# Optimization experiments

Measured on AMD Instinct MI355X. Metric: run time of the kernel, lower is better.

## Reference

```python
import jax, jax.numpy as jnp
import numpy as np

D_MODEL = 1024
NUM_HEADS = 16
HEAD_DIM = D_MODEL // NUM_HEADS  # 64
THETA = 10000.0
B, S = 2, 2048


def setup_inputs() -> dict:
    key = jax.random.key(0)
    k1, k2, k3 = jax.random.split(key, 3)
    sigma_qkv = (2.0 / (D_MODEL + 3 * D_MODEL)) ** 0.5
    sigma_o = (2.0 / (D_MODEL + D_MODEL)) ** 0.5
    x = jax.random.normal(k1, (B, S, D_MODEL), dtype=jnp.float32)
    w_qkv = jax.random.normal(k2, (3 * D_MODEL, D_MODEL), dtype=jnp.float32) * sigma_qkv
    w_o = jax.random.normal(k3, (D_MODEL, D_MODEL), dtype=jnp.float32) * sigma_o
    token_positions = jnp.arange(S, dtype=jnp.int32)
    return {"x": x, "w_qkv": w_qkv, "w_o": w_o, "token_positions": token_positions, "mask": 1}


def _rope(t, pos):
    # t: (B, H, S, HEAD_DIM); pos: (S,) int
    ids = jnp.arange(HEAD_DIM // 2, dtype=jnp.float32)
    freqs = pos.astype(jnp.float32)[:, None] * (THETA ** (-2.0 * ids / HEAD_DIM))  # (S, HEAD_DIM/2)
    cos, sin = jnp.cos(freqs), jnp.sin(freqs)
    even, odd = t[..., 0::2], t[..., 1::2]
    r_even = even * cos - odd * sin
    r_odd = odd * cos + even * sin
    # interleave back to original layout
    return jnp.stack([r_even, r_odd], axis=-1).reshape(t.shape)


def reference(x, w_qkv, w_o, token_positions, mask):
    # fused QKV projection: Linear computes x @ W^T with W [out, in]
    qkv = x @ w_qkv.T  # (B, S, 3*D_MODEL)
    q, k, v = jnp.split(qkv, 3, axis=-1)

    def to_heads(t):
        return t.reshape(B, S, NUM_HEADS, HEAD_DIM).transpose(0, 2, 1, 3)  # (B, H, S, Dh)

    q, k, v = to_heads(q), to_heads(k), to_heads(v)
    q = _rope(q, token_positions)
    k = _rope(k, token_positions)

    scores = jnp.einsum('bhqd,bhkd->bhqk', q, k)
    if mask:  # causal: lower-triangular allowed
        causal = jnp.tril(jnp.ones((S, S), dtype=bool))
        scores = jnp.where(causal, scores, -jnp.inf)
    attn = jax.nn.softmax(scores * (HEAD_DIM ** -0.5), axis=-1)
    out = jnp.einsum('bhqk,bhkd->bhqd', attn, v)  # (B, H, S, Dh)
    out = out.transpose(0, 2, 1, 3).reshape(B, S, D_MODEL)
    return out @ w_o.T
```

## Files before the change

kernel.cpp:

```cpp
#include <hip/hip_runtime.h>
#include <hip/hip_bf16.h>
#include <math.h>

typedef __bf16 bf16_t;
typedef __bf16 bf16x8 __attribute__((ext_vector_type(8)));
typedef __bf16 bf16x4 __attribute__((ext_vector_type(4)));
typedef float  f32x4  __attribute__((ext_vector_type(4)));

#define D_MODEL 1024
#define NH      16
#define HD      64
#define BATCH   2
#define SEQ     2048
#define MROWS   (BATCH*SEQ)
#define QKVN    (3*D_MODEL)
#define FA_PAD  72
#define SCALE_LOG2E 0.18033688011112042f

__device__ __forceinline__ void async_cp16(const bf16_t* g, bf16_t* l) {
    __builtin_amdgcn_global_load_lds(
        (const __attribute__((address_space(1))) void*)g,
        (__attribute__((address_space(3))) void*)l,
        16, 0, 0);
}

__global__ void cvt_all(const float* __restrict__ x, const float* __restrict__ wq,
                        const float* __restrict__ wo,
                        bf16_t* __restrict__ xb, bf16_t* __restrict__ wqb,
                        bf16_t* __restrict__ wob) {
    const int nx = MROWS * D_MODEL, nq = QKVN * D_MODEL;
    int i = (blockIdx.x * blockDim.x + threadIdx.x) * 4;
    const float* s; bf16_t* d; int off;
    if (i < nx)           { s = x;  d = xb;  off = i; }
    else if (i < nx + nq) { s = wq; d = wqb; off = i - nx; }
    else                  { s = wo; d = wob; off = i - nx - nq; }
    float4 v = *(const float4*)(s + off);
    d[off]     = (bf16_t)v.x;
    d[off + 1] = (bf16_t)v.y;
    d[off + 2] = (bf16_t)v.z;
    d[off + 3] = (bf16_t)v.w;
}

template <typename OutT, int NI>
__global__ __launch_bounds__(256) void gemm_nt(const bf16_t* __restrict__ A,
                                               const bf16_t* __restrict__ Bm,
                                               OutT* __restrict__ C,
                                               int M, int N, int K) {
    __shared__ __align__(16) bf16_t As[2][128 * 32];
    __shared__ __align__(16) bf16_t Bs[2][NI * 32 * 32];
    const int tid  = threadIdx.x;
    const int w    = tid >> 6;
    const int lane = tid & 63;
    const int quad = lane >> 4;
    const int l16  = lane & 15;
    const int m0   = blockIdx.x * 128;
    const int n0   = blockIdx.y * (NI * 32);
    const int wm   = (w >> 1) * 64;
    const int wn   = (w & 1) * (NI * 16);

    f32x4 acc[4][NI];
    #pragma unroll
    for (int i = 0; i < 4; i++)
        #pragma unroll
        for (int j = 0; j < NI; j++)
            acc[i][j] = (f32x4){0.f, 0.f, 0.f, 0.f};

    const bf16_t* Ag0 = A  + (size_t)(m0 + (tid >> 2)) * K + (tid & 3) * 8;
    const bf16_t* Ag1 = Ag0 + (size_t)64 * K;
    const bf16_t* Bg0 = Bm + (size_t)(n0 + (tid >> 2)) * K + (tid & 3) * 8;
    const bf16_t* Bg1 = Bg0 + (size_t)64 * K;

    for (int k0 = 0; k0 < K; k0 += 64) {
        #pragma unroll
        for (int kk = 0; kk < 2; kk++) {
            const int kc = k0 + kk * 32;
            async_cp16(Ag0 + kc, &As[kk][(size_t)tid * 8]);
            async_cp16(Ag1 + kc, &As[kk][((size_t)tid + 256) * 8]);
            async_cp16(Bg0 + kc, &Bs[kk][(size_t)tid * 8]);
            if (NI == 4) async_cp16(Bg1 + kc, &Bs[kk][((size_t)tid + 256) * 8]);
        }
        __syncthreads();

        #pragma unroll
        for (int kk = 0; kk < 2; kk++) {
            bf16x8 af[4], bfr[NI];
            #pragma unroll
            for (int mi = 0; mi < 4; mi++)
                af[mi] = *(const bf16x8*)&As[kk][(wm + mi * 16 + l16) * 32 + quad * 8];
            #pragma unroll
            for (int ni = 0; ni < NI; ni++)
                bfr[ni] = *(const bf16x8*)&Bs[kk][(wn + ni * 16 + l16) * 32 + quad * 8];
            #pragma unroll
            for (int mi = 0; mi < 4; mi++)
                #pragma unroll
                for (int ni = 0; ni < NI; ni++)
                    acc[mi][ni] = __builtin_amdgcn_mfma_f32_16x16x32_bf16(
                        af[mi], bfr[ni], acc[mi][ni], 0, 0, 0);
        }
        __syncthreads();
    }

    #pragma unroll
    for (int mi = 0; mi < 4; mi++)
        #pragma unroll
        for (int ni = 0; ni < NI; ni++) {
            const int col = n0 + wn + ni * 16 + l16;
            #pragma unroll
            for (int r = 0; r < 4; r++) {
                const int row = m0 + wm + mi * 16 + quad * 4 + r;
                C[(size_t)row * N + col] = (OutT)acc[mi][ni][r];
            }
        }
}

__global__ __launch_bounds__(256) void rope_split(const bf16_t* __restrict__ qkv,
                                                  const int* __restrict__ pos,
                                                  bf16_t* __restrict__ Qh,
                                                  bf16_t* __restrict__ Kh,
                                                  bf16_t* __restrict__ VT) {
    __shared__ bf16_t vs[128][FA_PAD];
    const int tid   = threadIdx.x;
    const int s_loc = tid >> 1;
    const int half  = tid & 1;
    const int s0    = blockIdx.x * 128;
    const int bh    = blockIdx.y;
    const int b     = bh >> 4, h = bh & 15;
    const int s     = s0 + s_loc;

    const bf16_t* row = qkv + (size_t)(b * SEQ + s) * QKVN + h * HD + half * 32;

    bf16_t qbuf[32], kbuf[32], vbuf[32];
    #pragma unroll
    for (int j = 0; j < 4; j++) {
        *(bf16x8*)&qbuf[j * 8] = *(const bf16x8*)(row + j * 8);
        *(bf16x8*)&kbuf[j * 8] = *(const bf16x8*)(row + D_MODEL + j * 8);
        *(bf16x8*)&vbuf[j * 8] = *(const bf16x8*)(row + 2 * D_MODEL + j * 8);
    }

    const float pf = (float)pos[s];
    #pragma unroll
    for (int p = 0; p < 16; p++) {
        const int d2 = half * 16 + p;
        const float inv = __expf(-0.28782313662425575f * (float)d2);
        const float f = pf * inv;
        const float c = cosf(f), sn = sinf(f);
        float qe = (float)qbuf[2 * p], qo = (float)qbuf[2 * p + 1];
        float ke = (float)kbuf[2 * p], ko = (float)kbuf[2 * p + 1];
        qbuf[2 * p]     = (bf16_t)(qe * c - qo * sn);
        qbuf[2 * p + 1] = (bf16_t)(qo * c + qe * sn);
        kbuf[2 * p]     = (bf16_t)(ke * c - ko * sn);
        kbuf[2 * p + 1] = (bf16_t)(ko * c + ke * sn);
    }

    bf16_t* qdst = Qh + ((size_t)bh * SEQ + s) * HD + half * 32;
    bf16_t* kdst = Kh + ((size_t)bh * SEQ + s) * HD + half * 32;
    #pragma unroll
    for (int j = 0; j < 4; j++) {
        *(bf16x8*)(qdst + j * 8) = *(bf16x8*)&qbuf[j * 8];
        *(bf16x8*)(kdst + j * 8) = *(bf16x8*)&kbuf[j * 8];
        *(bf16x8*)&vs[s_loc][half * 32 + j * 8] = *(bf16x8*)&vbuf[j * 8];
    }
    __syncthreads();

    const int d  = tid >> 2;
    const int sc = tid & 3;
    bf16_t tmp[32];
    #pragma unroll
    for (int i = 0; i < 32; i++) tmp[i] = vs[sc * 32 + i][d];
    bf16_t* vdst = VT + ((size_t)bh * HD + d) * SEQ + s0 + sc * 32;
    #pragma unroll
    for (int j = 0; j < 4; j++)
        *(bf16x8*)(vdst + j * 8) = *(bf16x8*)&tmp[j * 8];
}

__global__ __launch_bounds__(512) void flash_attn(const bf16_t* __restrict__ Qh,
                                                  const bf16_t* __restrict__ Kh,
                                                  const bf16_t* __restrict__ VT,
                                                  bf16_t* __restrict__ AO) {
    __shared__ __align__(16) bf16_t Vs[2][64 * FA_PAD];
    __shared__ __align__(16) bf16_t pT[8][16][FA_PAD];

    const int tid  = threadIdx.x;
    const int w    = tid >> 6;
    const int lane = tid & 63;
    const int quad = lane >> 4;
    const int l16  = lane & 15;
    const int wq   = w & 3;
    const int g    = w >> 2;

    const int bid  = blockIdx.x;
    const int xcd  = bid & 7;
    const int mm   = bid >> 3;
    const int bh   = (mm >> 4) * 8 + xcd;
    const int pair = mm & 15;
    const int qt_big = 31 - pair;
    const int my_qt  = g ? pair : qt_big;
    const int niter  = qt_big + 1;

    const bf16_t* Qb = Qh + (size_t)bh * SEQ * HD;
    const bf16_t* Kb = Kh + (size_t)bh * SEQ * HD;
    const bf16_t* Vb = VT + (size_t)bh * HD * SEQ;

    const int q0 = my_qt * 64 + wq * 16;
    const bf16x8 aq0 = *(const bf16x8*)(Qb + (size_t)(q0 + l16) * HD + quad * 8);
    const bf16x8 aq1 = *(const bf16x8*)(Qb + (size_t)(q0 + l16) * HD + 32 + quad * 8);

    const int srow = tid >> 3, scol = (tid & 7) * 8;
    const int lds_off = srow * FA_PAD + scol;

    f32x4 o[4];
    #pragma unroll
    for (int i = 0; i < 4; i++) o[i] = (f32x4){0.f, 0.f, 0.f, 0.f};
    float lsum = 0.f;

    bf16x8 pV = *(const bf16x8*)(Vb + (size_t)srow * SEQ + scol);
    *(bf16x8*)&Vs[0][lds_off] = pV;

    for (int kt = 0; kt < niter; ++kt) {
        const int cur = kt & 1;
        if (kt + 1 < niter) {
            const int kn = (kt + 1) * 64;
            pV = *(const bf16x8*)(Vb + (size_t)srow * SEQ + kn + scol);
        }
        __syncthreads();

        if (kt <= my_qt) {
            const int k0 = kt * 64;
            const bool diag = (kt == my_qt);
            const bf16_t* VsC = &Vs[cur][0];

            #pragma unroll
            for (int ni = 0; ni < 4; ni++) {
                if (diag && ni > wq) {
                    *(bf16x4*)&pT[w][l16][ni * 16 + quad * 4] = (bf16x4){0, 0, 0, 0};
                    continue;
                }
                const bf16_t* kp = Kb + (size_t)(k0 + ni * 16 + l16) * HD + quad * 8;
                bf16x8 kb0 = *(const bf16x8*)kp;
                bf16x8 kb1 = *(const bf16x8*)(kp + 32);
                f32x4 t = (f32x4){0.f, 0.f, 0.f, 0.f};
                t = __builtin_amdgcn_mfma_f32_16x16x32_bf16(kb0, aq0, t, 0, 0, 0);
                t = __builtin_amdgcn_mfma_f32_16x16x32_bf16(kb1, aq1, t, 0, 0, 0);
                bf16x4 pk;
                #pragma unroll
                for (int r = 0; r < 4; r++) {
                    float pv = exp2f(t[r] * SCALE_LOG2E);
                    if (diag && (ni * 16 + quad * 4 + r > wq * 16 + l16)) pv = 0.f;
                    lsum += pv;
                    pk[r] = (bf16_t)pv;
                }
                *(bf16x4*)&pT[w][l16][ni * 16 + quad * 4] = pk;
            }

            #pragma unroll
            for (int ks = 0; ks < 2; ks++) {
                if (diag && wq * 16 + 15 < ks * 32) continue;
                bf16x8 ap = *(const bf16x8*)&pT[w][l16][ks * 32 + quad * 8];
                #pragma unroll
                for (int ni = 0; ni < 4; ni++) {
                    bf16x8 vb = *(const bf16x8*)&VsC[(ni * 16 + l16) * FA_PAD + ks * 32 + quad * 8];
                    o[ni] = __builtin_amdgcn_mfma_f32_16x16x32_bf16(ap, vb, o[ni], 0, 0, 0);
                }
            }
        }

        if (kt + 1 < niter)
            *(bf16x8*)&Vs[cur ^ 1][lds_off] = pV;
    }

    lsum += __shfl_xor(lsum, 16);
    lsum += __shfl_xor(lsum, 32);
    f32x4 linv;
    #pragma unroll
    for (int r = 0; r < 4; r++)
        linv[r] = 1.0f / __shfl(lsum, quad * 4 + r);

    const int b = bh >> 4, h = bh & 15;
    #pragma unroll
    for (int ni = 0; ni < 4; ni++) {
        #pragma unroll
        for (int r = 0; r < 4; r++) {
            const size_t row = (size_t)b * SEQ + q0 + quad * 4 + r;
            AO[row * D_MODEL + h * HD + ni * 16 + l16] = (bf16_t)(o[ni][r] * linv[r]);
        }
    }
}

extern "C" void kernel_launch(void* const* d_in, const int* in_sizes, int n_in,
                              void* d_out, int out_size, void* d_ws, size_t ws_size,
                              hipStream_t stream) {
    const float* x     = (const float*)d_in[0];
    const float* w_qkv = (const float*)d_in[1];
    const float* w_o   = (const float*)d_in[2];
    const int*   tpos  = (const int*)d_in[3];
    float*       out   = (float*)d_out;

    char* ws = (char*)d_ws;
    bf16_t* xb  = (bf16_t*)(ws);
    bf16_t* wqb = (bf16_t*)(ws + 8388608);
    bf16_t* wob = (bf16_t*)(ws + 14680064);
    bf16_t* qkv = (bf16_t*)(ws + 16777216);
    bf16_t* Qh  = (bf16_t*)(ws + 41943040);
    bf16_t* Kh  = (bf16_t*)(ws + 50331648);
    bf16_t* VT  = (bf16_t*)(ws + 58720256);
    bf16_t* AO  = (bf16_t*)(ws + 67108864);

    cvt_all<<<8192, 256, 0, stream>>>(x, w_qkv, w_o, xb, wqb, wob);

    gemm_nt<bf16_t, 4><<<dim3(32, 24), 256, 0, stream>>>(xb, wqb, qkv, MROWS, QKVN, D_MODEL);

    rope_split<<<dim3(SEQ / 128, BATCH * NH), 256, 0, stream>>>(qkv, tpos, Qh, Kh, VT);

    flash_attn<<<512, 512, 0, stream>>>(Qh, Kh, VT, AO);

    gemm_nt<float, 2><<<dim3(32, 16), 256, 0, stream>>>(AO, wob, out, MROWS, D_MODEL, D_MODEL);
}
```

Before: 224.7 us.

## Fuse RoPE and head split into QKV GEMM epilogue; stage K tiles in LDS

The QKV projection GEMM now applies RoPE in its epilogue, using a lane shuffle to fetch each even/odd partner. It writes Q and K straight into head-major layout and V transposed, which removes the intermediate qkv buffer and the separate rope_split kernel. Flash attention now double-buffers K tiles in LDS alongside V instead of reading K fragments directly from global memory on every iteration. The trade-off is that the epilogue stores are scattered 2-byte writes, uncoalesced for VT in particular, and cos/sin are recomputed per element. The extra K buffers also raise LDS use in flash attention.

```diff
diff --git a/kernel.cpp b/kernel.cpp
--- a/kernel.cpp
+++ b/kernel.cpp
@@ -39,6 +39,107 @@
     d[off + 1] = (bf16_t)v.y;
     d[off + 2] = (bf16_t)v.z;
     d[off + 3] = (bf16_t)v.w;
+}
+
+__global__ __launch_bounds__(256) void gemm_qkv_rope(const bf16_t* __restrict__ A,
+                                                     const bf16_t* __restrict__ Bm,
+                                                     const int* __restrict__ pos,
+                                                     bf16_t* __restrict__ Qh,
+                                                     bf16_t* __restrict__ Kh,
+                                                     bf16_t* __restrict__ VT) {
+    const int K = D_MODEL, N = QKVN;
+    __shared__ __align__(16) bf16_t As[2][128 * 32];
+    __shared__ __align__(16) bf16_t Bs[2][128 * 32];
+    const int tid  = threadIdx.x;
+    const int w    = tid >> 6;
+    const int lane = tid & 63;
+    const int quad = lane >> 4;
+    const int l16  = lane & 15;
+    const int m0   = blockIdx.x * 128;
+    const int n0   = blockIdx.y * 128;
+    const int wm   = (w >> 1) * 64;
+    const int wn   = (w & 1) * 64;
+
+    f32x4 acc[4][4];
+    #pragma unroll
+    for (int i = 0; i < 4; i++)
+        #pragma unroll
+        for (int j = 0; j < 4; j++)
+            acc[i][j] = (f32x4){0.f, 0.f, 0.f, 0.f};
+
+    const bf16_t* Ag0 = A  + (size_t)(m0 + (tid >> 2)) * K + (tid & 3) * 8;
+    const bf16_t* Ag1 = Ag0 + (size_t)64 * K;
+    const bf16_t* Bg0 = Bm + (size_t)(n0 + (tid >> 2)) * K + (tid & 3) * 8;
+    const bf16_t* Bg1 = Bg0 + (size_t)64 * K;
+
+    for (int k0 = 0; k0 < K; k0 += 64) {
+        #pragma unroll
+        for (int kk = 0; kk < 2; kk++) {
+            const int kc = k0 + kk * 32;
+            async_cp16(Ag0 + kc, &As[kk][(size_t)tid * 8]);
+            async_cp16(Ag1 + kc, &As[kk][((size_t)tid + 256) * 8]);
+            async_cp16(Bg0 + kc, &Bs[kk][(size_t)tid * 8]);
+            async_cp16(Bg1 + kc, &Bs[kk][((size_t)tid + 256) * 8]);
+        }
+        __syncthreads();
+
+        #pragma unroll
+        for (int kk = 0; kk < 2; kk++) {
+            bf16x8 af[4], bfr[4];
+            #pragma unroll
+            for (int mi = 0; mi < 4; mi++)
+                af[mi] = *(const bf16x8*)&As[kk][(wm + mi * 16 + l16) * 32 + quad * 8];
+            #pragma unroll
+            for (int ni = 0; ni < 4; ni++)
+                bfr[ni] = *(const bf16x8*)&Bs[kk][(wn + ni * 16 + l16) * 32 + quad * 8];
+            #pragma unroll
+            for (int mi = 0; mi < 4; mi++)
+                #pragma unroll
+                for (int ni = 0; ni < 4; ni++)
+                    acc[mi][ni] = __builtin_amdgcn_mfma_f32_16x16x32_bf16(
+                        af[mi], bfr[ni], acc[mi][ni], 0, 0, 0);
+        }
+        __syncthreads();
+    }
+
+    #pragma unroll
+    for (int ni = 0; ni < 4; ni++) {
+        const int col    = n0 + wn + ni * 16 + l16;
+        const int region = col >> 10;
+        const int c10    = col & 1023;
+        const int h      = c10 >> 6;
+        const int d      = c10 & 63;
+        if (region < 2) {
+            bf16_t* dst = region ? Kh : Qh;
+            const int d2 = d >> 1;
+            const float sgn = (col & 1) ? 1.f : -1.f;
+            const float inv = __expf(-0.28782313662425575f * (float)d2);
+            #pragma unroll
+            for (int mi = 0; mi < 4; mi++) {
+                #pragma unroll
+                for (int r = 0; r < 4; r++) {
+                    const int row = m0 + wm + mi * 16 + quad * 4 + r;
+                    const int s = row & (SEQ - 1), bb = row >> 11;
+                    const float f = (float)pos[s] * inv;
+                    const float c = cosf(f), sn = sinf(f);
+                    const float val  = acc[mi][ni][r];
+                    const float pair = __shfl_xor(val, 1);
+                    dst[((size_t)(bb * NH + h) * SEQ + s) * HD + d] =
+                        (bf16_t)(val * c + sgn * pair * sn);
+                }
+            }
+        } else {
+            #pragma unroll
+            for (int mi = 0; mi < 4; mi++) {
+                #pragma unroll
+                for (int r = 0; r < 4; r++) {
+                    const int row = m0 + wm + mi * 16 + quad * 4 + r;
+                    const int s = row & (SEQ - 1), bb = row >> 11;
+                    VT[((size_t)(bb * NH + h) * HD + d) * SEQ + s] = (bf16_t)acc[mi][ni][r];
+                }
+            }
+        }
+    }
 }
 
 template <typename OutT, int NI>
@@ -113,70 +214,11 @@
         }
 }
 
-__global__ __launch_bounds__(256) void rope_split(const bf16_t* __restrict__ qkv,
-                                                  const int* __restrict__ pos,
-                                                  bf16_t* __restrict__ Qh,
-                                                  bf16_t* __restrict__ Kh,
-                                                  bf16_t* __restrict__ VT) {
-    __shared__ bf16_t vs[128][FA_PAD];
-    const int tid   = threadIdx.x;
-    const int s_loc = tid >> 1;
-    const int half  = tid & 1;
-    const int s0    = blockIdx.x * 128;
-    const int bh    = blockIdx.y;
-    const int b     = bh >> 4, h = bh & 15;
-    const int s     = s0 + s_loc;
-
-    const bf16_t* row = qkv + (size_t)(b * SEQ + s) * QKVN + h * HD + half * 32;
-
-    bf16_t qbuf[32], kbuf[32], vbuf[32];
-    #pragma unroll
-    for (int j = 0; j < 4; j++) {
-        *(bf16x8*)&qbuf[j * 8] = *(const bf16x8*)(row + j * 8);
-        *(bf16x8*)&kbuf[j * 8] = *(const bf16x8*)(row + D_MODEL + j * 8);
-        *(bf16x8*)&vbuf[j * 8] = *(const bf16x8*)(row + 2 * D_MODEL + j * 8);
-    }
-
-    const float pf = (float)pos[s];
-    #pragma unroll
-    for (int p = 0; p < 16; p++) {
-        const int d2 = half * 16 + p;
-        const float inv = __expf(-0.28782313662425575f * (float)d2);
-        const float f = pf * inv;
-        const float c = cosf(f), sn = sinf(f);
-        float qe = (float)qbuf[2 * p], qo = (float)qbuf[2 * p + 1];
-        float ke = (float)kbuf[2 * p], ko = (float)kbuf[2 * p + 1];
-        qbuf[2 * p]     = (bf16_t)(qe * c - qo * sn);
-        qbuf[2 * p + 1] = (bf16_t)(qo * c + qe * sn);
-        kbuf[2 * p]     = (bf16_t)(ke * c - ko * sn);
-        kbuf[2 * p + 1] = (bf16_t)(ko * c + ke * sn);
-    }
-
-    bf16_t* qdst = Qh + ((size_t)bh * SEQ + s) * HD + half * 32;
-    bf16_t* kdst = Kh + ((size_t)bh * SEQ + s) * HD + half * 32;
-    #pragma unroll
-    for (int j = 0; j < 4; j++) {
-        *(bf16x8*)(qdst + j * 8) = *(bf16x8*)&qbuf[j * 8];
-        *(bf16x8*)(kdst + j * 8) = *(bf16x8*)&kbuf[j * 8];
-        *(bf16x8*)&vs[s_loc][half * 32 + j * 8] = *(bf16x8*)&vbuf[j * 8];
-    }
-    __syncthreads();
-
-    const int d  = tid >> 2;
-    const int sc = tid & 3;
-    bf16_t tmp[32];
-    #pragma unroll
-    for (int i = 0; i < 32; i++) tmp[i] = vs[sc * 32 + i][d];
-    bf16_t* vdst = VT + ((size_t)bh * HD + d) * SEQ + s0 + sc * 32;
-    #pragma unroll
-    for (int j = 0; j < 4; j++)
-        *(bf16x8*)(vdst + j * 8) = *(bf16x8*)&tmp[j * 8];
-}
-
 __global__ __launch_bounds__(512) void flash_attn(const bf16_t* __restrict__ Qh,
                                                   const bf16_t* __restrict__ Kh,
                                                   const bf16_t* __restrict__ VT,
                                                   bf16_t* __restrict__ AO) {
+    __shared__ __align__(16) bf16_t Ks[2][64 * FA_PAD];
     __shared__ __align__(16) bf16_t Vs[2][64 * FA_PAD];
     __shared__ __align__(16) bf16_t pT[8][16][FA_PAD];
 
@@ -213,20 +255,23 @@
     for (int i = 0; i < 4; i++) o[i] = (f32x4){0.f, 0.f, 0.f, 0.f};
     float lsum = 0.f;
 
+    bf16x8 pK = *(const bf16x8*)(Kb + (size_t)srow * HD + scol);
     bf16x8 pV = *(const bf16x8*)(Vb + (size_t)srow * SEQ + scol);
+    *(bf16x8*)&Ks[0][lds_off] = pK;
     *(bf16x8*)&Vs[0][lds_off] = pV;
 
     for (int kt = 0; kt < niter; ++kt) {
         const int cur = kt & 1;
         if (kt + 1 < niter) {
             const int kn = (kt + 1) * 64;
+            pK = *(const bf16x8*)(Kb + (size_t)(kn + srow) * HD + scol);
             pV = *(const bf16x8*)(Vb + (size_t)srow * SEQ + kn + scol);
         }
         __syncthreads();
 
         if (kt <= my_qt) {
-            const int k0 = kt * 64;
             const bool diag = (kt == my_qt);
+            const bf16_t* KsC = &Ks[cur][0];
             const bf16_t* VsC = &Vs[cur][0];
 
             #pragma unroll
@@ -235,9 +280,8 @@
                     *(bf16x4*)&pT[w][l16][ni * 16 + quad * 4] = (bf16x4){0, 0, 0, 0};
                     continue;
                 }
-                const bf16_t* kp = Kb + (size_t)(k0 + ni * 16 + l16) * HD + quad * 8;
-                bf16x8 kb0 = *(const bf16x8*)kp;
-                bf16x8 kb1 = *(const bf16x8*)(kp + 32);
+                bf16x8 kb0 = *(const bf16x8*)&KsC[(ni * 16 + l16) * FA_PAD + quad * 8];
+                bf16x8 kb1 = *(const bf16x8*)&KsC[(ni * 16 + l16) * FA_PAD + 32 + quad * 8];
                 f32x4 t = (f32x4){0.f, 0.f, 0.f, 0.f};
                 t = __builtin_amdgcn_mfma_f32_16x16x32_bf16(kb0, aq0, t, 0, 0, 0);
                 t = __builtin_amdgcn_mfma_f32_16x16x32_bf16(kb1, aq1, t, 0, 0, 0);
@@ -264,8 +308,10 @@
             }
         }
 
-        if (kt + 1 < niter)
+        if (kt + 1 < niter) {
+            *(bf16x8*)&Ks[cur ^ 1][lds_off] = pK;
             *(bf16x8*)&Vs[cur ^ 1][lds_off] = pV;
+        }
     }
 
     lsum += __shfl_xor(lsum, 16);
@@ -299,7 +345,6 @@
     bf16_t* xb  = (bf16_t*)(ws);
     bf16_t* wqb = (bf16_t*)(ws + 8388608);
     bf16_t* wob = (bf16_t*)(ws + 14680064);
-    bf16_t* qkv = (bf16_t*)(ws + 16777216);
     bf16_t* Qh  = (bf16_t*)(ws + 41943040);
     bf16_t* Kh  = (bf16_t*)(ws + 50331648);
     bf16_t* VT  = (bf16_t*)(ws + 58720256);
@@ -307,9 +352,7 @@
 
     cvt_all<<<8192, 256, 0, stream>>>(x, w_qkv, w_o, xb, wqb, wob);
 
-    gemm_nt<bf16_t, 4><<<dim3(32, 24), 256, 0, stream>>>(xb, wqb, qkv, MROWS, QKVN, D_MODEL);
-
-    rope_split<<<dim3(SEQ / 128, BATCH * NH), 256, 0, stream>>>(qkv, tpos, Qh, Kh, VT);
+    gemm_qkv_rope<<<dim3(32, 24), 256, 0, stream>>>(xb, wqb, tpos, Qh, Kh, VT);
 
     flash_attn<<<512, 512, 0, stream>>>(Qh, Kh, VT, AO);
 
```

Measured after the change: 295.4 us. 1.31x slower.
